# Kernel tuning notes

Measured on AMD Instinct MI355X. Metric: run time of the kernel, lower is better.

The kernel has to match this reference:

```python
import jax, jax.numpy as jnp
import numpy as np

N = 50000   # nodes
E = 600000  # edges (avg degree 12)
D = 128     # feature dim (input_dim == output_dim for residual)
G = 8       # graphs in batch
EPS = 1e-5


def setup_inputs() -> dict:
    key = jax.random.key(0)
    ks = jax.random.split(key, 8)
    x = jax.random.normal(ks[0], (N, D), dtype=jnp.float32)
    edge_index = jax.random.randint(ks[1], (2, E), 0, N)
    batch = jnp.sort(jax.random.randint(ks[2], (N,), 0, G))
    s = 1.0 / np.sqrt(D)
    Wl = jax.random.normal(ks[3], (D, D), dtype=jnp.float32) * s
    bl = jax.random.normal(ks[4], (D,), dtype=jnp.float32) * s
    Wr = jax.random.normal(ks[5], (D, D), dtype=jnp.float32) * s
    return {
        "x": x,
        "edge_index": edge_index,
        "batch": batch,
        "num_graphs": G,
        "Wl": Wl,
        "bl": bl,
        "Wr": Wr,
        "gn_weight": jnp.ones((D,), jnp.float32),
        "gn_bias": jnp.zeros((D,), jnp.float32),
        "mean_scale": jnp.ones((D,), jnp.float32),
    }


def reference(x, edge_index, batch, num_graphs, Wl, bl, Wr, gn_weight, gn_bias, mean_scale):
    n = x.shape[0]
    src, dst = edge_index[0], edge_index[1]

    # SAGEConv: mean-aggregate neighbor (source) features at target nodes
    ones_e = jnp.ones(src.shape[0], dtype=x.dtype)
    deg = jax.ops.segment_sum(ones_e, dst, num_segments=n)          # [N]
    agg = jax.ops.segment_sum(x[src], dst, num_segments=n)          # [N, D]
    agg = agg / jnp.maximum(deg, 1.0)[:, None]
    f = agg @ Wl.T + bl + x @ Wr.T                                  # lin_l(agg) + lin_r(x)

    # exact (erf) GELU, as torch F.gelu default
    f = jax.nn.gelu(f, approximate=False)

    # GraphNorm: per-graph statistics with learnable mean_scale
    ones_n = jnp.ones(n, dtype=x.dtype)
    cnt = jax.ops.segment_sum(ones_n, batch, num_segments=num_graphs)[:, None]  # [G,1]
    mean = jax.ops.segment_sum(f, batch, num_segments=num_graphs) / cnt         # [G,D]
    out = f - mean_scale * mean[batch]
    var = jax.ops.segment_sum(out * out, batch, num_segments=num_graphs) / cnt  # [G,D]
    out = out / jnp.sqrt(var[batch] + EPS) * gn_weight + gn_bias

    # dropout is identity in eval mode; residual add
    return out + x
```

## Files before the change

kernel.cpp:

```cpp
#include <hip/hip_runtime.h>

#define D 128
#define NGRAPH 8
#define EPS 1e-5f
#define CAP 48

typedef __attribute__((ext_vector_type(4))) float f32x4;
typedef __attribute__((ext_vector_type(2))) float f32x2;
typedef __attribute__((ext_vector_type(8))) short s16x8;

__device__ __forceinline__ unsigned short f2bf(float f) {
    unsigned int u = __float_as_uint(f);
    u += 0x7fffu + ((u >> 16) & 1u);
    return (unsigned short)(u >> 16);
}
__device__ __forceinline__ float blo(unsigned int u) { return __uint_as_float(u << 16); }
__device__ __forceinline__ float bhi(unsigned int u) { return __uint_as_float(u & 0xffff0000u); }

__global__ __launch_bounds__(256) void prep_fill_kernel(
    const float* __restrict__ Wl, const float* __restrict__ Wr,
    unsigned short* __restrict__ Bsw,
    const float* __restrict__ x, unsigned int* __restrict__ xb,
    unsigned int* __restrict__ xf8,
    const int* __restrict__ batch, int* __restrict__ bnd,
    const int* __restrict__ ei, int* __restrict__ cnt, int* __restrict__ adj,
    int N, int E, int Npad, int fillB)
{
    int b = blockIdx.x;
    if (b < 128) {
        int t = b * 256 + threadIdx.x;
        int j    = t & 7;
        int ln   = (t >> 3) & 63;
        int ks   = (t >> 9) & 7;
        int tile = t >> 12;
        int k = ks * 32 + (ln >> 4) * 8 + j;
        int d = tile * 16 + (ln & 15);
        float v = (k < 128) ? Wl[(size_t)d * 128 + k] : Wr[(size_t)d * 128 + (k - 128)];
        Bsw[t] = f2bf(v);
    } else if (b == 128) {
        int g = threadIdx.x;
        if (g <= NGRAPH) {
            int lo = 0, hi = N;
            while (lo < hi) {
                int mid = (lo + hi) >> 1;
                if (batch[mid] < g) lo = mid + 1; else hi = mid;
            }
            bnd[g] = lo;
        }
    } else if (b < 129 + fillB) {
        int e = (b - 129) * 256 + threadIdx.x;
        if (e < E) {
            int dst = ei[E + e];
            int pos = atomicAdd(&cnt[dst], 1);
            if (pos < CAP) adj[(size_t)dst * CAP + pos] = ei[e];
        }
    } else {
        int iu = (b - 129 - fillB) * 256 + threadIdx.x;
        if (iu < Npad * 32) {
            int n = iu >> 5, slot = iu & 31;
            if (iu < N * 32) {
                float4 p = *(const float4*)(x + (size_t)iu * 4);
                uint2 o;
                o.x = (unsigned int)f2bf(p.x) | ((unsigned int)f2bf(p.y) << 16);
                o.y = (unsigned int)f2bf(p.z) | ((unsigned int)f2bf(p.w) << 16);
                *(uint2*)(xb + (size_t)iu * 2) = o;
                int u8 = __builtin_amdgcn_cvt_pk_fp8_f32(p.x, p.y, 0, false);
                u8     = __builtin_amdgcn_cvt_pk_fp8_f32(p.z, p.w, u8, true);
                xf8[(size_t)n * 32 + slot] = (unsigned int)u8;
            } else {
                *(uint2*)(xb + (size_t)iu * 2) = make_uint2(0u, 0u);
                xf8[(size_t)n * 32 + slot] = 0u;
            }
        }
    }
}

__global__ __launch_bounds__(256, 8) void fused_kernel(
    const unsigned short* __restrict__ xf8, const int* __restrict__ cnt,
    const int* __restrict__ adj,
    const unsigned short* __restrict__ xb16, const unsigned short* __restrict__ Bsw,
    const float* __restrict__ bl, const int* __restrict__ batch,
    float* __restrict__ gsum, float* __restrict__ gsumsq,
    unsigned short* __restrict__ fout16, int N)
{
    __shared__ unsigned int aggL[32][68];

    int wave = threadIdx.x >> 6, lane = threadIdx.x & 63;
    int nblk0 = blockIdx.x * 32;

#pragma unroll
    for (int s = 0; s < 8; ++s) {
        int ln = wave * 8 + s;
        int node = nblk0 + ln;
        int dg = (node < N) ? cnt[node] : 0;
        int lm = dg < CAP ? dg : CAP;
        int v = (lane < lm) ? adj[(size_t)node * CAP + lane] : 0;
        float a0 = 0.0f, a1 = 0.0f;
        int i = 0;
        for (; i + 8 <= lm; i += 8) {
            int nb[8];
#pragma unroll
            for (int k = 0; k < 8; ++k) nb[k] = __shfl(v, i + k, 64);
            unsigned short u[8];
#pragma unroll
            for (int k = 0; k < 8; ++k) u[k] = xf8[(size_t)nb[k] * 64 + lane];
#pragma unroll
            for (int k = 0; k < 8; ++k) {
                f32x2 d2 = __builtin_amdgcn_cvt_pk_f32_fp8((int)(unsigned int)u[k], false);
                a0 += d2[0]; a1 += d2[1];
            }
        }
        for (; i < lm; ++i) {
            int nb = __shfl(v, i, 64);
            f32x2 d2 = __builtin_amdgcn_cvt_pk_f32_fp8(
                (int)(unsigned int)xf8[(size_t)nb * 64 + lane], false);
            a0 += d2[0]; a1 += d2[1];
        }
        float iv = 1.0f / (float)(dg > 0 ? dg : 1);
        aggL[ln][lane] =
            (unsigned int)f2bf(a0 * iv) | ((unsigned int)f2bf(a1 * iv) << 16);
    }
    __syncthreads();

    int row0 = nblk0 + (wave >> 1) * 16;
    int th = wave & 1;
    int m = lane & 15, quad = lane >> 4;
    int r = row0 + m;
    int lr = (wave >> 1) * 16 + m;

    s16x8 afrag[8];
#pragma unroll
    for (int ks = 0; ks < 4; ++ks)
        afrag[ks] = *(const s16x8*)&aggL[lr][ks * 16 + quad * 4];
    const unsigned short* xp = xb16 + (size_t)r * 128 + quad * 8;
#pragma unroll
    for (int ks = 0; ks < 4; ++ks) afrag[4 + ks] = *(const s16x8*)(xp + ks * 32);

    int nbase = row0;
    bool uni = (nbase + 15 < N) && (batch[nbase] == batch[nbase + 15]);
    int gu = (nbase < N) ? batch[nbase] : 0;

#pragma unroll
    for (int t = 0; t < 4; ++t) {
        int tile = th * 4 + t;
        f32x4 acc = {0.0f, 0.0f, 0.0f, 0.0f};
        const s16x8* bptr = (const s16x8*)Bsw + (size_t)(tile * 8) * 64 + lane;
#pragma unroll
        for (int ks = 0; ks < 8; ++ks)
            acc = __builtin_amdgcn_mfma_f32_16x16x32_bf16(afrag[ks], bptr[(size_t)ks * 64], acc, 0, 0, 0);
        int d = tile * 16 + m;
        float bias = bl[d];
        float sm = 0.0f, sq = 0.0f;
#pragma unroll
        for (int rr = 0; rr < 4; ++rr) {
            int node = nbase + quad * 4 + rr;
            float v = acc[rr] + bias;
            float g = 0.5f * v * (1.0f + erff(v * 0.70710678118654752f));
            if (node < N) {
                fout16[(size_t)node * 128 + d] = f2bf(g);
                if (uni) { sm += g; sq += g * g; }
                else {
                    int gg = batch[node];
                    unsafeAtomicAdd(&gsum[gg * D + d], g);
                    unsafeAtomicAdd(&gsumsq[gg * D + d], g * g);
                }
            }
        }
        if (uni) {
            sm += __shfl_xor(sm, 16, 64); sm += __shfl_xor(sm, 32, 64);
            sq += __shfl_xor(sq, 16, 64); sq += __shfl_xor(sq, 32, 64);
            if (quad == 0) {
                unsafeAtomicAdd(&gsum[gu * D + d], sm);
                unsafeAtomicAdd(&gsumsq[gu * D + d], sq);
            }
        }
    }
}

__global__ __launch_bounds__(256) void final_kernel(
    const unsigned int* __restrict__ f16, const float* __restrict__ x,
    const int* __restrict__ batch, const int* __restrict__ bnd,
    const float* __restrict__ gsum, const float* __restrict__ gsumsq,
    const float* __restrict__ ms,
    const float* __restrict__ gw, const float* __restrict__ gb,
    float* __restrict__ out, int N)
{
    int t = blockIdx.x * 256 + threadIdx.x;
    if (t >= N * (D / 4)) return;
    int n  = t >> 5;
    int d0 = (t & 31) * 4;
    int g  = batch[n];
    int c  = bnd[g + 1] - bnd[g];
    float invc = 1.0f / (float)(c > 0 ? c : 1);
    size_t row = (size_t)n * D + d0;
    uint2 fu = *(const uint2*)(f16 + (size_t)n * 64 + (d0 >> 1));
    float4 fv = make_float4(blo(fu.x), bhi(fu.x), blo(fu.y), bhi(fu.y));
    float4 xv = *(const float4*)(x + row);
    float4 s1 = *(const float4*)(gsum + g * D + d0);
    float4 s2 = *(const float4*)(gsumsq + g * D + d0);
    float4 msv = *(const float4*)(ms + d0);
    float4 gwv = *(const float4*)(gw + d0);
    float4 gbv = *(const float4*)(gb + d0);
    float4 o;
    {
        float mu = s1.x * invc, q = s2.x * invc, a = msv.x * mu;
        float sc = rsqrtf(q - 2.0f * a * mu + a * a + EPS);
        o.x = (fv.x - a) * sc * gwv.x + gbv.x + xv.x;
    }
    {
        float mu = s1.y * invc, q = s2.y * invc, a = msv.y * mu;
        float sc = rsqrtf(q - 2.0f * a * mu + a * a + EPS);
        o.y = (fv.y - a) * sc * gwv.y + gbv.y + xv.y;
    }
    {
        float mu = s1.z * invc, q = s2.z * invc, a = msv.z * mu;
        float sc = rsqrtf(q - 2.0f * a * mu + a * a + EPS);
        o.z = (fv.z - a) * sc * gwv.z + gbv.z + xv.z;
    }
    {
        float mu = s1.w * invc, q = s2.w * invc, a = msv.w * mu;
        float sc = rsqrtf(q - 2.0f * a * mu + a * a + EPS);
        o.w = (fv.w - a) * sc * gwv.w + gbv.w + xv.w;
    }
    *(float4*)(out + row) = o;
}

extern "C" void kernel_launch(void* const* d_in, const int* in_sizes, int n_in,
                              void* d_out, int out_size, void* d_ws, size_t ws_size,
                              hipStream_t stream)
{
    const float* x     = (const float*)d_in[0];
    const int*   ei    = (const int*)d_in[1];
    const int*   batch = (const int*)d_in[2];
    const float* Wl = (const float*)d_in[4];
    const float* bl = (const float*)d_in[5];
    const float* Wr = (const float*)d_in[6];
    const float* gw = (const float*)d_in[7];
    const float* gb = (const float*)d_in[8];
    const float* ms = (const float*)d_in[9];
    float* out = (float*)d_out;

    int N = in_sizes[0] / D;
    int E = in_sizes[1] / 2;
    int NBLK = (N + 63) / 64;
    int Npad = NBLK * 64;
    int NB32 = Npad / 32;

    unsigned int*   fout16 = (unsigned int*)d_ws;
    unsigned int*   xf8  = fout16 + (size_t)Npad * 64;
    unsigned int*   xb   = xf8 + (size_t)Npad * 32;
    unsigned short* Bsw  = (unsigned short*)(xb + (size_t)Npad * 64);
    float* gsum   = (float*)(Bsw + 32768);
    float* gsumsq = gsum + NGRAPH * D;
    unsigned int* pad = (unsigned int*)(gsumsq + NGRAPH * D);
    int*   cnt    = (int*)(pad + 4);
    int*   bnd    = cnt + N;
    int*   adj    = bnd + (NGRAPH + 1);

    hipMemsetAsync(gsum, 0,
                   (2 * NGRAPH * D) * sizeof(float) + 4 * sizeof(unsigned int)
                   + (size_t)N * sizeof(int), stream);

    int fillB = (E + 255) / 256;
    int xbB   = (Npad * 32 + 255) / 256;
    prep_fill_kernel<<<129 + fillB + xbB, 256, 0, stream>>>(
        Wl, Wr, Bsw, x, xb, xf8, batch, bnd, ei, cnt, adj, N, E, Npad, fillB);

    fused_kernel<<<NB32, 256, 0, stream>>>(
        (const unsigned short*)xf8, cnt, adj,
        (const unsigned short*)xb, Bsw, bl, batch,
        gsum, gsumsq, (unsigned short*)fout16, N);

    {
        int threads = N * (D / 4);
        final_kernel<<<(threads + 255) / 256, 256, 0, stream>>>(
            fout16, x, batch, bnd, gsum, gsumsq, ms, gw, gb, out, N);
    }
}
```

Measured before the change: 184.0 us.

## Bin edges per 32-node block and aggregate via LDS float atomics

Replaces the per-node adjacency list (one atomic per destination node, capped at 48 neighbours) with per-block edge bins holding packed (src, local dst) entries. The fused kernel walks its bin edge by edge and accumulates fp8-decoded features into a float LDS tile with shared-memory atomics, then normalises by an LDS degree count before converting to bf16 for the MFMA. The aim is fewer scattered global atomics and less per-node imbalance, at the cost of LDS atomic traffic and a larger LDS footprint that may reduce occupancy. Packing src into 16 bits assumes node indices below 65536, and the bin capacity of 512 silently drops edges if a bin overflows.

```diff
diff --git a/kernel.cpp b/kernel.cpp
--- a/kernel.cpp
+++ b/kernel.cpp
@@ -3,7 +3,7 @@
 #define D 128
 #define NGRAPH 8
 #define EPS 1e-5f
-#define CAP 48
+#define BINCAP 512
 
 typedef __attribute__((ext_vector_type(4))) float f32x4;
 typedef __attribute__((ext_vector_type(2))) float f32x2;
@@ -23,7 +23,8 @@
     const float* __restrict__ x, unsigned int* __restrict__ xb,
     unsigned int* __restrict__ xf8,
     const int* __restrict__ batch, int* __restrict__ bnd,
-    const int* __restrict__ ei, int* __restrict__ cnt, int* __restrict__ adj,
+    const int* __restrict__ ei, unsigned int* __restrict__ bcnt,
+    unsigned int* __restrict__ bbuf,
     int N, int E, int Npad, int fillB)
 {
     int b = blockIdx.x;
@@ -51,8 +52,12 @@
         int e = (b - 129) * 256 + threadIdx.x;
         if (e < E) {
             int dst = ei[E + e];
-            int pos = atomicAdd(&cnt[dst], 1);
-            if (pos < CAP) adj[(size_t)dst * CAP + pos] = ei[e];
+            int src = ei[e];
+            int bin = dst >> 5;
+            unsigned int pos = atomicAdd(&bcnt[(size_t)bin * 16], 1u);
+            if (pos < BINCAP)
+                bbuf[(size_t)bin * BINCAP + pos] =
+                    (unsigned int)src | ((unsigned int)(dst & 31) << 16);
         }
     } else {
         int iu = (b - 129 - fillB) * 256 + threadIdx.x;
@@ -76,49 +81,40 @@
 }
 
 __global__ __launch_bounds__(256, 8) void fused_kernel(
-    const unsigned short* __restrict__ xf8, const int* __restrict__ cnt,
-    const int* __restrict__ adj,
+    const unsigned short* __restrict__ xf8,
+    const unsigned int* __restrict__ bcnt, const unsigned int* __restrict__ bbuf,
     const unsigned short* __restrict__ xb16, const unsigned short* __restrict__ Bsw,
     const float* __restrict__ bl, const int* __restrict__ batch,
     float* __restrict__ gsum, float* __restrict__ gsumsq,
     unsigned short* __restrict__ fout16, int N)
 {
-    __shared__ unsigned int aggL[32][68];
+    __shared__ float aggF[32][132];
+    __shared__ int degL[32];
 
     int wave = threadIdx.x >> 6, lane = threadIdx.x & 63;
-    int nblk0 = blockIdx.x * 32;
-
-#pragma unroll
-    for (int s = 0; s < 8; ++s) {
-        int ln = wave * 8 + s;
-        int node = nblk0 + ln;
-        int dg = (node < N) ? cnt[node] : 0;
-        int lm = dg < CAP ? dg : CAP;
-        int v = (lane < lm) ? adj[(size_t)node * CAP + lane] : 0;
-        float a0 = 0.0f, a1 = 0.0f;
-        int i = 0;
-        for (; i + 8 <= lm; i += 8) {
-            int nb[8];
-#pragma unroll
-            for (int k = 0; k < 8; ++k) nb[k] = __shfl(v, i + k, 64);
-            unsigned short u[8];
-#pragma unroll
-            for (int k = 0; k < 8; ++k) u[k] = xf8[(size_t)nb[k] * 64 + lane];
-#pragma unroll
-            for (int k = 0; k < 8; ++k) {
-                f32x2 d2 = __builtin_amdgcn_cvt_pk_f32_fp8((int)(unsigned int)u[k], false);
-                a0 += d2[0]; a1 += d2[1];
-            }
-        }
-        for (; i < lm; ++i) {
-            int nb = __shfl(v, i, 64);
+    int bin = blockIdx.x;
+    int nblk0 = bin * 32;
+
+    for (int k = threadIdx.x; k < 32 * 132; k += 256) ((float*)aggF)[k] = 0.0f;
+    if (threadIdx.x < 32) degL[threadIdx.x] = 0;
+    __syncthreads();
+
+    {
+        int ec = (int)bcnt[(size_t)bin * 16];
+        if (ec > BINCAP) ec = BINCAP;
+        const unsigned int* bb = bbuf + (size_t)bin * BINCAP;
+        unsigned int entn = (wave < ec) ? bb[wave] : 0u;
+        for (int e = wave; e < ec; e += 4) {
+            unsigned int ent = entn;
+            if (e + 4 < ec) entn = bb[e + 4];
+            int src = ent & 0xffff;
+            int dl  = ent >> 16;
             f32x2 d2 = __builtin_amdgcn_cvt_pk_f32_fp8(
-                (int)(unsigned int)xf8[(size_t)nb * 64 + lane], false);
-            a0 += d2[0]; a1 += d2[1];
-        }
-        float iv = 1.0f / (float)(dg > 0 ? dg : 1);
-        aggL[ln][lane] =
-            (unsigned int)f2bf(a0 * iv) | ((unsigned int)f2bf(a1 * iv) << 16);
+                (int)(unsigned int)xf8[(size_t)src * 64 + lane], false);
+            atomicAdd(&aggF[dl][2 * lane], d2[0]);
+            atomicAdd(&aggF[dl][2 * lane + 1], d2[1]);
+            if (lane == 0) atomicAdd(&degL[dl], 1);
+        }
     }
     __syncthreads();
 
@@ -128,10 +124,18 @@
     int r = row0 + m;
     int lr = (wave >> 1) * 16 + m;
 
+    int dg = degL[lr];
+    float inv = 1.0f / (float)(dg > 0 ? dg : 1);
+
     s16x8 afrag[8];
 #pragma unroll
-    for (int ks = 0; ks < 4; ++ks)
-        afrag[ks] = *(const s16x8*)&aggL[lr][ks * 16 + quad * 4];
+    for (int ks = 0; ks < 4; ++ks) {
+        const float* ap = &aggF[lr][ks * 32 + quad * 8];
+        s16x8 a;
+#pragma unroll
+        for (int j = 0; j < 8; ++j) a[j] = (short)f2bf(ap[j] * inv);
+        afrag[ks] = a;
+    }
     const unsigned short* xp = xb16 + (size_t)r * 128 + quad * 8;
 #pragma unroll
     for (int ks = 0; ks < 4; ++ks) afrag[4 + ks] = *(const s16x8*)(xp + ks * 32);
@@ -252,22 +256,22 @@
     unsigned short* Bsw  = (unsigned short*)(xb + (size_t)Npad * 64);
     float* gsum   = (float*)(Bsw + 32768);
     float* gsumsq = gsum + NGRAPH * D;
-    unsigned int* pad = (unsigned int*)(gsumsq + NGRAPH * D);
-    int*   cnt    = (int*)(pad + 4);
-    int*   bnd    = cnt + N;
-    int*   adj    = bnd + (NGRAPH + 1);
+    unsigned int* pad  = (unsigned int*)(gsumsq + NGRAPH * D);
+    unsigned int* bcnt = pad + 4;
+    int*          bnd  = (int*)(bcnt + (size_t)NB32 * 16);
+    unsigned int* bbuf = (unsigned int*)(bnd + (NGRAPH + 1));
 
     hipMemsetAsync(gsum, 0,
                    (2 * NGRAPH * D) * sizeof(float) + 4 * sizeof(unsigned int)
-                   + (size_t)N * sizeof(int), stream);
+                   + (size_t)NB32 * 16 * sizeof(unsigned int), stream);
 
     int fillB = (E + 255) / 256;
     int xbB   = (Npad * 32 + 255) / 256;
     prep_fill_kernel<<<129 + fillB + xbB, 256, 0, stream>>>(
-        Wl, Wr, Bsw, x, xb, xf8, batch, bnd, ei, cnt, adj, N, E, Npad, fillB);
+        Wl, Wr, Bsw, x, xb, xf8, batch, bnd, ei, bcnt, bbuf, N, E, Npad, fillB);
 
     fused_kernel<<<NB32, 256, 0, stream>>>(
-        (const unsigned short*)xf8, cnt, adj,
+        (const unsigned short*)xf8, bcnt, bbuf,
         (const unsigned short*)xb, Bsw, bl, batch,
         gsum, gsumsq, (unsigned short*)fout16, N);
 
```

Result: slower. 608.3 us (+230.7%).
